# Kernel tuning notes

Measured on AMD Instinct MI355X. Metric: run time of the kernel, lower is better.

The kernel has to match this reference:

```python
import jax, jax.numpy as jnp
import numpy as np

B, T, I, H = 65536, 9, 57, 2  # batch, seq_len, input_size, hidden_size


def setup_inputs() -> dict:
    key = jax.random.key(0)
    ks = jax.random.split(key, 7)
    return {
        "x": jax.random.normal(ks[0], (B, T, I), dtype=jnp.float32),
        "W_ih": jax.random.normal(ks[1], (4 * H, I), dtype=jnp.float32) * 0.1,
        "W_hh": jax.random.normal(ks[2], (4 * H, H), dtype=jnp.float32) * 0.1,
        "b_ih": jax.random.normal(ks[3], (4 * H,), dtype=jnp.float32) * 0.1,
        "b_hh": jax.random.normal(ks[4], (4 * H,), dtype=jnp.float32) * 0.1,
        "fc_w": jax.random.normal(ks[5], (1, H), dtype=jnp.float32) * 0.1,
        "fc_b": jax.random.normal(ks[6], (1,), dtype=jnp.float32) * 0.1,
    }


def reference(x, W_ih, W_hh, b_ih, b_hh, fc_w, fc_b):
    # Precompute input contribution to the gates for all timesteps: [B, T, 4H]
    gx = jnp.einsum("bti,gi->btg", x, W_ih) + b_ih + b_hh
    h0 = jnp.zeros((x.shape[0], W_hh.shape[1]), dtype=x.dtype)
    c0 = jnp.zeros_like(h0)

    def step(carry, g_t):
        h, c = carry
        g = g_t + h @ W_hh.T  # [B, 4H]
        i, f, gg, o = jnp.split(g, 4, axis=-1)  # PyTorch gate order: i, f, g, o
        i = jax.nn.sigmoid(i)
        f = jax.nn.sigmoid(f)
        gg = jnp.tanh(gg)
        o = jax.nn.sigmoid(o)
        c = f * c + i * gg
        h = o * jnp.tanh(c)
        return (h, c), None

    (h_T, _), _ = jax.lax.scan(step, (h0, c0), jnp.swapaxes(gx, 0, 1))  # scan over time
    # fc applied to last hidden state: [B, 1]
    return h_T @ fc_w.T + fc_b
```

## Files before the change

### kernel.cpp

```cpp
#include <hip/hip_runtime.h>


#define B_TOTAL 65536
#define T_STEPS 9
#define I_DIM   57
#define NROWS   (B_TOTAL * T_STEPS)
#define P1_BLOCKS 1152
#define NGROUPS  (P1_BLOCKS * 32)
#define ROWS_PER_GROUP (NROWS / NGROUPS)

__device__ __forceinline__ float fast_tanh(float v) {
    float e = __builtin_amdgcn_exp2f(2.885390082f * v);
    return 1.0f - 2.0f * __builtin_amdgcn_rcpf(e + 1.0f);
}
__device__ __forceinline__ float fast_sig(float v) {
    return 0.5f * fast_tanh(0.5f * v) + 0.5f;
}


#define LOADX(BUF, R) do {                                                  \
    const float* xr_ = x + (size_t)(R) * I_DIM;                             \
    _Pragma("unroll")                                                       \
    for (int k = 0; k < 7; ++k) BUF[k] = xr_[j + 8 * k];                    \
    BUF[7] = xr_[56];   \
} while (0)

#define PROCESS(BUF, R) do {                                                \
    float acc_[8];                                                          \
    _Pragma("unroll")                                                       \
    for (int d = 0; d < 8; ++d) {                                           \
        float s_ = wrot[d][0] * BUF[0];                                     \
        _Pragma("unroll")                                                   \
        for (int k = 1; k < 8; ++k) s_ += wrot[d][k] * BUF[k];              \
        acc_[d] = s_;                                                       \
    }                                                                       \
    float tot_ = acc_[0];                                                   \
    _Pragma("unroll")                                                       \
    for (int d = 1; d < 8; ++d) tot_ += __shfl(acc_[d], (j - d) & 7, 8);    \
    tot_ += bsum;                                                           \
    const int r_ = (R);                                                     \
    const int b_ = r_ / T_STEPS;                                            \
    const int t_ = r_ - b_ * T_STEPS;                                       \
    gxT[((size_t)t_ * B_TOTAL + b_) * 8 + j] = tot_;                        \
} while (0)

__global__ __launch_bounds__(256, 2)
void lstm_gx(const float* __restrict__ x,
             const float* __restrict__ W_ih,
             const float* __restrict__ b_ih,
             const float* __restrict__ b_hh,
             float* __restrict__ gxT) {
    const int lane = threadIdx.x & 63;
    const int j    = lane & 7;
    const int grp  = (blockIdx.x * 256 + threadIdx.x) >> 3;

    float wrot[8][8];
#pragma unroll
    for (int d = 0; d < 8; ++d) {
        const int g = (j + d) & 7;
        const float* wr = W_ih + g * I_DIM;
#pragma unroll
        for (int k = 0; k < 7; ++k) wrot[d][k] = wr[j + 8 * k];
        wrot[d][7] = (j == 0) ? wr[56] : 0.0f;
    }
    float bsum = b_ih[j] + b_hh[j];
#pragma unroll
    for (int d = 0; d < 8; ++d)
#pragma unroll
        for (int k = 0; k < 8; ++k)
            asm volatile("" : "+v"(wrot[d][k]));

#define ROW(IT) ((IT) * NGROUPS + grp)

    float xa[8], xb[8];
    LOADX(xa, ROW(0));
#pragma unroll
    for (int it = 0; it < ROWS_PER_GROUP; it += 2) {
        if (it + 1 < ROWS_PER_GROUP) LOADX(xb, ROW(it + 1));
        PROCESS(xa, ROW(it));
        if (it + 2 < ROWS_PER_GROUP) LOADX(xa, ROW(it + 2));
        if (it + 1 < ROWS_PER_GROUP) PROCESS(xb, ROW(it + 1));
    }
#undef ROW
}


__global__ __launch_bounds__(256, 2)
void lstm_rec(const float* __restrict__ gxT,
              const float* __restrict__ W_hh,
              const float* __restrict__ fc_w,
              const float* __restrict__ fc_b,
              float* __restrict__ out) {
    const int b = blockIdx.x * 256 + threadIdx.x;

    float w0[8], w1[8];
#pragma unroll
    for (int g = 0; g < 8; ++g) { w0[g] = W_hh[g * 2]; w1[g] = W_hh[g * 2 + 1]; }

    float h0 = 0.f, h1 = 0.f, c0 = 0.f, c1 = 0.f;

    const float* gb0 = gxT + (size_t)b * 8;
    float4 ga = *(const float4*)(gb0);
    float4 gbv = *(const float4*)(gb0 + 4);

#pragma unroll
    for (int t = 0; t < T_STEPS; ++t) {
        float4 na, nb;
        if (t + 1 < T_STEPS) {
            const float* p = gxT + ((size_t)(t + 1) * B_TOTAL + b) * 8;
            na = *(const float4*)(p);
            nb = *(const float4*)(p + 4);
        }
        const float i0 = fast_sig (ga.x + h0 * w0[0] + h1 * w1[0]);
        const float i1 = fast_sig (ga.y + h0 * w0[1] + h1 * w1[1]);
        const float f0 = fast_sig (ga.z + h0 * w0[2] + h1 * w1[2]);
        const float f1 = fast_sig (ga.w + h0 * w0[3] + h1 * w1[3]);
        const float g0 = fast_tanh(gbv.x + h0 * w0[4] + h1 * w1[4]);
        const float g1 = fast_tanh(gbv.y + h0 * w0[5] + h1 * w1[5]);
        const float o0 = fast_sig (gbv.z + h0 * w0[6] + h1 * w1[6]);
        const float o1 = fast_sig (gbv.w + h0 * w0[7] + h1 * w1[7]);
        c0 = f0 * c0 + i0 * g0;
        c1 = f1 * c1 + i1 * g1;
        h0 = o0 * fast_tanh(c0);
        h1 = o1 * fast_tanh(c1);
        if (t + 1 < T_STEPS) { ga = na; gbv = nb; }
    }

    out[b] = h0 * fc_w[0] + h1 * fc_w[1] + fc_b[0];
}

extern "C" void kernel_launch(void* const* d_in, const int* in_sizes, int n_in,
                              void* d_out, int out_size, void* d_ws, size_t ws_size,
                              hipStream_t stream) {
    const float* x    = (const float*)d_in[0];
    const float* W_ih = (const float*)d_in[1];
    const float* W_hh = (const float*)d_in[2];
    const float* b_ih = (const float*)d_in[3];
    const float* b_hh = (const float*)d_in[4];
    const float* fc_w = (const float*)d_in[5];
    const float* fc_b = (const float*)d_in[6];
    float* out = (float*)d_out;
    float* gxT = (float*)d_ws;

    lstm_gx<<<dim3(P1_BLOCKS), dim3(256), 0, stream>>>(x, W_ih, b_ih, b_hh, gxT);
    lstm_rec<<<dim3(B_TOTAL / 256), dim3(256), 0, stream>>>(gxT, W_hh, fc_w, fc_b, out);
}
```

Baseline: 41.35 us.

## Stage x chunks through double-buffered LDS with coalesced float4 loads

The input-projection kernel now loads 64-row chunks of x with coalesced float4 global loads into a double-buffered shared-memory tile, overlapping the next chunk's load with compute on the current one. Previously each 8-lane group read a row with strided scalar loads. The gx workspace layout changes from time-major to batch-major, so the recurrence kernel reads each sequence contiguously. Launch-bounds occupancy hints are dropped and the kernel adds block-wide barriers and LDS traffic, where the row stride of 57 may cause bank conflicts.

Result: slower. 42.52 us (+2.8%).

```diff
diff --git a/kernel.cpp b/kernel.cpp
--- a/kernel.cpp
+++ b/kernel.cpp
@@ -5,9 +5,11 @@
 #define T_STEPS 9
 #define I_DIM   57
 #define NROWS   (B_TOTAL * T_STEPS)
-#define P1_BLOCKS 1152
-#define NGROUPS  (P1_BLOCKS * 32)
-#define ROWS_PER_GROUP (NROWS / NGROUPS)
+#define CHUNK_ROWS 64
+#define CHUNK_DW   (CHUNK_ROWS * I_DIM)
+#define CHUNK_F4   (CHUNK_DW / 4)
+#define CHUNKS_PER_BLOCK 4
+#define P1_BLOCKS  (NROWS / CHUNK_ROWS / CHUNKS_PER_BLOCK)
 
 __device__ __forceinline__ float fast_tanh(float v) {
     float e = __builtin_amdgcn_exp2f(2.885390082f * v);
@@ -18,41 +20,17 @@
 }
 
 
-#define LOADX(BUF, R) do {                                                  \
-    const float* xr_ = x + (size_t)(R) * I_DIM;                             \
-    _Pragma("unroll")                                                       \
-    for (int k = 0; k < 7; ++k) BUF[k] = xr_[j + 8 * k];                    \
-    BUF[7] = xr_[56];   \
-} while (0)
-
-#define PROCESS(BUF, R) do {                                                \
-    float acc_[8];                                                          \
-    _Pragma("unroll")                                                       \
-    for (int d = 0; d < 8; ++d) {                                           \
-        float s_ = wrot[d][0] * BUF[0];                                     \
-        _Pragma("unroll")                                                   \
-        for (int k = 1; k < 8; ++k) s_ += wrot[d][k] * BUF[k];              \
-        acc_[d] = s_;                                                       \
-    }                                                                       \
-    float tot_ = acc_[0];                                                   \
-    _Pragma("unroll")                                                       \
-    for (int d = 1; d < 8; ++d) tot_ += __shfl(acc_[d], (j - d) & 7, 8);    \
-    tot_ += bsum;                                                           \
-    const int r_ = (R);                                                     \
-    const int b_ = r_ / T_STEPS;                                            \
-    const int t_ = r_ - b_ * T_STEPS;                                       \
-    gxT[((size_t)t_ * B_TOTAL + b_) * 8 + j] = tot_;                        \
-} while (0)
-
-__global__ __launch_bounds__(256, 2)
+__global__ __launch_bounds__(256)
 void lstm_gx(const float* __restrict__ x,
              const float* __restrict__ W_ih,
              const float* __restrict__ b_ih,
              const float* __restrict__ b_hh,
-             float* __restrict__ gxT) {
-    const int lane = threadIdx.x & 63;
-    const int j    = lane & 7;
-    const int grp  = (blockIdx.x * 256 + threadIdx.x) >> 3;
+             float* __restrict__ gx) {
+    __shared__ float lds[2][CHUNK_DW];
+
+    const int tid = threadIdx.x;
+    const int j   = tid & 7;
+    const int grp = tid >> 3;
 
     float wrot[8][8];
 #pragma unroll
@@ -70,23 +48,71 @@
         for (int k = 0; k < 8; ++k)
             asm volatile("" : "+v"(wrot[d][k]));
 
-#define ROW(IT) ((IT) * NGROUPS + grp)
+    const int c0 = blockIdx.x * CHUNKS_PER_BLOCK;
 
-    float xa[8], xb[8];
-    LOADX(xa, ROW(0));
+    float4 st0, st1, st2, st3;
+
+#define STAGE_LOAD(C) do {                                                  \
+        const float4* xc_ = (const float4*)(x + (size_t)(C) * CHUNK_DW);    \
+        st0 = xc_[tid];                                                     \
+        st1 = xc_[256 + tid];                                               \
+        st2 = xc_[512 + tid];                                               \
+        if (tid < CHUNK_F4 - 768) st3 = xc_[768 + tid];                     \
+    } while (0)
+
+#define STAGE_WRITE(S) do {                                                 \
+        float4* L_ = (float4*)lds[S];                                       \
+        L_[tid] = st0;                                                      \
+        L_[256 + tid] = st1;                                                \
+        L_[512 + tid] = st2;                                                \
+        if (tid < CHUNK_F4 - 768) L_[768 + tid] = st3;                      \
+    } while (0)
+
+#define COMPUTE(S, C) do {                                                  \
+        _Pragma("unroll")                                                   \
+        for (int iter = 0; iter < 2; ++iter) {                              \
+            const int rl_ = iter * 32 + grp;                                \
+            const float* row_ = lds[S] + rl_ * I_DIM;                       \
+            float xv_[8];                                                   \
+            _Pragma("unroll")                                               \
+            for (int k = 0; k < 7; ++k) xv_[k] = row_[j + 8 * k];           \
+            xv_[7] = row_[56];        \
+            float acc_[8];                                                  \
+            _Pragma("unroll")                                               \
+            for (int d = 0; d < 8; ++d) {                                   \
+                float s_ = wrot[d][0] * xv_[0];                             \
+                _Pragma("unroll")                                           \
+                for (int k = 1; k < 8; ++k) s_ += wrot[d][k] * xv_[k];      \
+                acc_[d] = s_;                                               \
+            }                                                               \
+            float tot_ = acc_[0];                                           \
+            _Pragma("unroll")                                               \
+            for (int d = 1; d < 8; ++d)                                     \
+                tot_ += __shfl(acc_[d], (j - d) & 7, 8);                    \
+            tot_ += bsum;                                                   \
+            const size_t R_ = (size_t)(C) * CHUNK_ROWS + rl_;               \
+            gx[R_ * 8 + j] = tot_;         \
+        }                                                                   \
+    } while (0)
+
+    STAGE_LOAD(c0);
+    STAGE_WRITE(0);
+
 #pragma unroll
-    for (int it = 0; it < ROWS_PER_GROUP; it += 2) {
-        if (it + 1 < ROWS_PER_GROUP) LOADX(xb, ROW(it + 1));
-        PROCESS(xa, ROW(it));
-        if (it + 2 < ROWS_PER_GROUP) LOADX(xa, ROW(it + 2));
-        if (it + 1 < ROWS_PER_GROUP) PROCESS(xb, ROW(it + 1));
+    for (int cc = 0; cc < CHUNKS_PER_BLOCK; ++cc) {
+        __syncthreads();
+        if (cc + 1 < CHUNKS_PER_BLOCK) STAGE_LOAD(c0 + cc + 1);
+        COMPUTE(cc & 1, c0 + cc);
+        if (cc + 1 < CHUNKS_PER_BLOCK) STAGE_WRITE((cc + 1) & 1);
     }
-#undef ROW
+#undef STAGE_LOAD
+#undef STAGE_WRITE
+#undef COMPUTE
 }
 
 
-__global__ __launch_bounds__(256, 2)
-void lstm_rec(const float* __restrict__ gxT,
+__global__ __launch_bounds__(256)
+void lstm_rec(const float* __restrict__ gx,
               const float* __restrict__ W_hh,
               const float* __restrict__ fc_w,
               const float* __restrict__ fc_b,
@@ -99,22 +125,22 @@
 
     float h0 = 0.f, h1 = 0.f, c0 = 0.f, c1 = 0.f;
 
-    const float* gb0 = gxT + (size_t)b * 8;
-    float4 ga = *(const float4*)(gb0);
-    float4 gbv = *(const float4*)(gb0 + 4);
+    const float* gb = gx + (size_t)b * (T_STEPS * 8);
+    float4 ga  = *(const float4*)(gb);
+    float4 gbv = *(const float4*)(gb + 4);
 
 #pragma unroll
     for (int t = 0; t < T_STEPS; ++t) {
         float4 na, nb;
         if (t + 1 < T_STEPS) {
-            const float* p = gxT + ((size_t)(t + 1) * B_TOTAL + b) * 8;
+            const float* p = gb + (t + 1) * 8;
             na = *(const float4*)(p);
             nb = *(const float4*)(p + 4);
         }
-        const float i0 = fast_sig (ga.x + h0 * w0[0] + h1 * w1[0]);
-        const float i1 = fast_sig (ga.y + h0 * w0[1] + h1 * w1[1]);
-        const float f0 = fast_sig (ga.z + h0 * w0[2] + h1 * w1[2]);
-        const float f1 = fast_sig (ga.w + h0 * w0[3] + h1 * w1[3]);
+        const float i0 = fast_sig (ga.x  + h0 * w0[0] + h1 * w1[0]);
+        const float i1 = fast_sig (ga.y  + h0 * w0[1] + h1 * w1[1]);
+        const float f0 = fast_sig (ga.z  + h0 * w0[2] + h1 * w1[2]);
+        const float f1 = fast_sig (ga.w  + h0 * w0[3] + h1 * w1[3]);
         const float g0 = fast_tanh(gbv.x + h0 * w0[4] + h1 * w1[4]);
         const float g1 = fast_tanh(gbv.y + h0 * w0[5] + h1 * w1[5]);
         const float o0 = fast_sig (gbv.z + h0 * w0[6] + h1 * w1[6]);
@@ -140,8 +166,8 @@
     const float* fc_w = (const float*)d_in[5];
     const float* fc_b = (const float*)d_in[6];
     float* out = (float*)d_out;
-    float* gxT = (float*)d_ws;
+    float* gx  = (float*)d_ws;
 
-    lstm_gx<<<dim3(P1_BLOCKS), dim3(256), 0, stream>>>(x, W_ih, b_ih, b_hh, gxT);
-    lstm_rec<<<dim3(B_TOTAL / 256), dim3(256), 0, stream>>>(gxT, W_hh, fc_w, fc_b, out);
+    lstm_gx<<<dim3(P1_BLOCKS), dim3(256), 0, stream>>>(x, W_ih, b_ih, b_hh, gx);
+    lstm_rec<<<dim3(B_TOTAL / 256), dim3(256), 0, stream>>>(gx, W_hh, fc_w, fc_b, out);
 }
```
